# Kernel tuning notes

Measured on AMD Instinct MI355X. Metric: run time of the kernel, lower is better.

The kernel has to match this reference:

```python
import jax, jax.numpy as jnp
import numpy as np

B, F, V, E = 16384, 20, 100000, 32
D_BOT = F * E            # 640
DIMS = (512, 256)        # bottom MLP dims
TDIMS = (128, 64)        # tower hidden dims
N_DOM = 4


def setup_inputs() -> dict:
    key = jax.random.key(0)
    ks = jax.random.split(key, 16)
    inp = {
        "feature_ids": jax.random.randint(ks[0], (B, F), 0, V, dtype=jnp.int64),
        "domain_id": jax.random.randint(ks[1], (B,), 0, N_DOM, dtype=jnp.int64),
        # embedding tables [F, V, E]
        "emb": jax.random.normal(ks[2], (F, V, E), dtype=jnp.float32) * 0.01,
        # bottom MLP: 640 -> 512 -> 256 (relu, no output layer)
        "W1": jax.random.normal(ks[3], (D_BOT, DIMS[0]), dtype=jnp.float32) * (1.0 / np.sqrt(D_BOT)),
        "b1": jnp.zeros((DIMS[0],), dtype=jnp.float32),
        "W2": jax.random.normal(ks[4], (DIMS[0], DIMS[1]), dtype=jnp.float32) * (1.0 / np.sqrt(DIMS[0])),
        "b2": jnp.zeros((DIMS[1],), dtype=jnp.float32),
        # towers (stacked over domain dim): 256 -> 128 -> 64 -> 1
        "TW1": jax.random.normal(ks[5], (N_DOM, DIMS[1], TDIMS[0]), dtype=jnp.float32) * (1.0 / np.sqrt(DIMS[1])),
        "Tb1": jnp.zeros((N_DOM, TDIMS[0]), dtype=jnp.float32),
        "TW2": jax.random.normal(ks[6], (N_DOM, TDIMS[0], TDIMS[1]), dtype=jnp.float32) * (1.0 / np.sqrt(TDIMS[0])),
        "Tb2": jnp.zeros((N_DOM, TDIMS[1]), dtype=jnp.float32),
        "TW3": jax.random.normal(ks[7], (N_DOM, TDIMS[1], 1), dtype=jnp.float32) * (1.0 / np.sqrt(TDIMS[1])),
        "Tb3": jnp.zeros((N_DOM, 1), dtype=jnp.float32),
    }
    return inp


def reference(feature_ids, domain_id, emb, W1, b1, W2, b2, TW1, Tb1, TW2, Tb2, TW3, Tb3):
    # Embedding lookup + concat: [B, F, E] -> [B, F*E]
    e = emb[jnp.arange(F)[None, :], feature_ids]          # [B, F, E]
    h = e.reshape(B, F * E)
    # Shared bottom MLP (relu)
    h = jax.nn.relu(h @ W1 + b1)                          # [B, 512]
    h = jax.nn.relu(h @ W2 + b2)                          # [B, 256]
    # All domain towers computed densely for every sample (faithful to source)
    t = jax.nn.relu(jnp.einsum('bi,dio->bdo', h, TW1) + Tb1[None])   # [B, D, 128]
    t = jax.nn.relu(jnp.einsum('bdi,dio->bdo', t, TW2) + Tb2[None])  # [B, D, 64]
    logit = jnp.einsum('bdi,dio->bdo', t, TW3) + Tb3[None]           # [B, D, 1]
    ys = jax.nn.sigmoid(logit)[..., 0]                    # [B, D]
    # Select per-sample domain output via mask (domains are exclusive)
    onehot = jax.nn.one_hot(domain_id, N_DOM, dtype=ys.dtype)        # [B, D]
    final = jnp.sum(ys * onehot, axis=1)                  # [B]
    return final
```

## Files before the change

### kernel.cpp

```cpp
#include <hip/hip_runtime.h>

#define B_SZ  16384
#define F_SZ  20
#define V_SZ  100000
#define E_SZ  32
#define DBOT  640
#define D1    512
#define D2    256
#define T1D   128
#define T2D   64
#define NDOM  4

typedef __bf16 bf16x8 __attribute__((ext_vector_type(8)));
typedef float  f32x4  __attribute__((ext_vector_type(4)));

#define MFMA(a, b, c) __builtin_amdgcn_mfma_f32_16x16x32_bf16((a), (b), (c), 0, 0, 0)

__global__ __launch_bounds__(256) void k_prep(const float* __restrict__ W1,
                                              const float* __restrict__ W2,
                                              const float* __restrict__ TW1,
                                              const float* __restrict__ TW2,
                                              __bf16* __restrict__ W1P,
                                              __bf16* __restrict__ W2P,
                                              __bf16* __restrict__ TW1P,
                                              __bf16* __restrict__ TW2P,
                                              int* __restrict__ cnt) {
  int bid = blockIdx.x, tid = threadIdx.x;
  const float* src; __bf16* dst; int n, k, N;
  if (bid < 160) {
    long g = (long)bid * 256 + tid;
    int lane = g & 63; int kkg = (int)((g >> 6) % 20); int ntile = (int)(g / 1280);
    n = ntile * 16 + (lane & 15); k = kkg * 32 + ((lane >> 4) << 3);
    src = W1; N = D1; dst = W1P + g * 8;
  } else if (bid < 224) {
    long g = (long)(bid - 160) * 256 + tid;
    int lane = g & 63; int kkg = (int)((g >> 6) & 15); int ntile = (int)(g >> 10);
    n = ntile * 16 + (lane & 15); k = kkg * 32 + ((lane >> 4) << 3);
    src = W2; N = D2; dst = W2P + g * 8;
  } else if (bid < 288) {
    long g = (long)(bid - 224) * 256 + tid;
    int d = (int)(g >> 12); long r = g & 4095;
    int lane = r & 63; int kkg = (int)((r >> 6) & 7); int ntile = (int)(r >> 9);
    n = ntile * 16 + (lane & 15); k = kkg * 32 + ((lane >> 4) << 3);
    src = TW1 + (long)d * D2 * T1D; N = T1D;
    dst = TW1P + ((long)(d * 64 + ntile * 8 + kkg) * 64 + lane) * 8;
  } else if (bid < 304) {
    long g = (long)(bid - 288) * 256 + tid;
    int d = (int)(g >> 10); long r = g & 1023;
    int lane = r & 63; int kkg = (int)((r >> 6) & 3); int ntile = (int)(r >> 8);
    n = ntile * 16 + (lane & 15); k = kkg * 32 + ((lane >> 4) << 3);
    src = TW2 + (long)d * T1D * T2D; N = T2D;
    dst = TW2P + ((long)(d * 16 + ntile * 4 + kkg) * 64 + lane) * 8;
  } else {
    if (tid < NDOM) cnt[tid] = 0;
    return;
  }
  bf16x8 o;
#pragma unroll
  for (int e = 0; e < 8; ++e) o[e] = (__bf16)src[(long)(k + e) * N + n];
  *(bf16x8*)dst = o;
}

__global__ __launch_bounds__(512) void k_fused(const int* __restrict__ fids,
                                               const int* __restrict__ dom,
                                               const float* __restrict__ emb,
                                               const __bf16* __restrict__ W1P,
                                               const float* __restrict__ b1,
                                               const __bf16* __restrict__ W2P,
                                               const float* __restrict__ b2,
                                               __bf16* __restrict__ h2,
                                               int* __restrict__ cnt,
                                               int* __restrict__ lists) {
  __shared__ int   ids_lds[64 * F_SZ];
  __shared__ __bf16 sA[2][64 * 64];
  __shared__ __bf16 h1[64 * D1];

  int bid = blockIdx.x, tid = threadIdx.x;
  int lane = tid & 63, w = tid >> 6;
  int lrow = lane & 15, kq = lane >> 4;
  int m0 = bid * 64;

  if (bid < 64 && tid < 256) {
    int i = bid * 256 + tid;
    int d = dom[i];
    int pl = tid & 63;
#pragma unroll
    for (int dd = 0; dd < NDOM; ++dd) {
      unsigned long long md = __ballot(d == dd);
      if (d == dd) {
        int myoff = __popcll(md & ((1ull << pl) - 1ull));
        int leader = __ffsll((long long)md) - 1;
        int base = 0;
        if (pl == leader) base = atomicAdd(&cnt[dd], __popcll(md));
        base = __shfl(base, leader);
        lists[dd * B_SZ + base + myoff] = i;
      }
    }
  }

  for (int i = tid; i < 64 * F_SZ; i += 512) ids_lds[i] = fids[m0 * F_SZ + i];
  __syncthreads();

  int srow = tid >> 3, sc = tid & 7;
  int sbyte = srow * 128 + ((sc ^ (srow & 7)) << 4);

  float4 g0, g1;
  {
    int f = sc >> 2;
    int id = ids_lds[srow * F_SZ + f];
    const float* p = emb + ((long)f * V_SZ + id) * E_SZ + ((sc & 3) << 3);
    g0 = *(const float4*)p; g1 = *(const float4*)(p + 4);
  }

  f32x4 acc[4][4] = {};

  for (int s = 0; s < 10; ++s) {
    bf16x8 o;
    o[0] = (__bf16)g0.x; o[1] = (__bf16)g0.y; o[2] = (__bf16)g0.z; o[3] = (__bf16)g0.w;
    o[4] = (__bf16)g1.x; o[5] = (__bf16)g1.y; o[6] = (__bf16)g1.z; o[7] = (__bf16)g1.w;
    *(bf16x8*)((char*)&sA[s & 1][0] + sbyte) = o;
    if (s < 9) {
      int f = 2 * (s + 1) + (sc >> 2);
      int id = ids_lds[srow * F_SZ + f];
      const float* p = emb + ((long)f * V_SZ + id) * E_SZ + ((sc & 3) << 3);
      g0 = *(const float4*)p; g1 = *(const float4*)(p + 4);
    }
    __syncthreads();

    const char* sAb = (const char*)&sA[s & 1][0];
#pragma unroll
    for (int kk = 0; kk < 2; ++kk) {
      bf16x8 af[4];
#pragma unroll
      for (int mi = 0; mi < 4; ++mi) {
        int byte = ((mi * 16 + lrow) * 128 + (kk * 32 + kq * 8) * 2) ^ ((lrow & 7) << 4);
        af[mi] = *(const bf16x8*)(sAb + byte);
      }
#pragma unroll
      for (int ni = 0; ni < 4; ++ni) {
        bf16x8 bfr = *(const bf16x8*)(W1P +
            ((long)((w * 4 + ni) * 20 + (s * 2 + kk)) * 64 + lane) * 8);
#pragma unroll
        for (int mi = 0; mi < 4; ++mi)
          acc[mi][ni] = MFMA(af[mi], bfr, acc[mi][ni]);
      }
    }
  }

#pragma unroll
  for (int ni = 0; ni < 4; ++ni) {
    int col = w * 64 + ni * 16 + lrow;
    float bv = b1[col];
#pragma unroll
    for (int mi = 0; mi < 4; ++mi) {
#pragma unroll
      for (int r = 0; r < 4; ++r) {
        int row = mi * 16 + kq * 4 + r;
        float v = acc[mi][ni][r] + bv;
        v = v > 0.f ? v : 0.f;
        int byte = (row * 1024 + col * 2) ^ ((row & 7) << 4);
        *(__bf16*)((char*)h1 + byte) = (__bf16)v;
      }
    }
  }
  __syncthreads();

  f32x4 acc2[4][2] = {};
  for (int kkg = 0; kkg < 16; ++kkg) {
    bf16x8 a2[4];
#pragma unroll
    for (int mi = 0; mi < 4; ++mi) {
      int byte = ((mi * 16 + lrow) * 1024 + kkg * 64 + kq * 16) ^ ((lrow & 7) << 4);
      a2[mi] = *(const bf16x8*)((const char*)h1 + byte);
    }
#pragma unroll
    for (int ni = 0; ni < 2; ++ni) {
      bf16x8 bfr = *(const bf16x8*)(W2P +
          ((long)((w * 2 + ni) * 16 + kkg) * 64 + lane) * 8);
#pragma unroll
      for (int mi = 0; mi < 4; ++mi)
        acc2[mi][ni] = MFMA(a2[mi], bfr, acc2[mi][ni]);
    }
  }

#pragma unroll
  for (int ni = 0; ni < 2; ++ni) {
    int col = w * 32 + ni * 16 + lrow;
    float bv = b2[col];
#pragma unroll
    for (int mi = 0; mi < 4; ++mi) {
#pragma unroll
      for (int r = 0; r < 4; ++r) {
        long row = m0 + mi * 16 + kq * 4 + r;
        float v = acc2[mi][ni][r] + bv;
        v = v > 0.f ? v : 0.f;
        h2[row * D2 + col] = (__bf16)v;
      }
    }
  }
}

__global__ __launch_bounds__(256) void k_tower(const __bf16* __restrict__ h2,
                                               const __bf16* __restrict__ TW1P,
                                               const __bf16* __restrict__ TW2P,
                                               const float* __restrict__ Tb1,
                                               const float* __restrict__ Tb2,
                                               const float* __restrict__ TW3,
                                               const float* __restrict__ Tb3,
                                               const int* __restrict__ cnt,
                                               const int* __restrict__ lists,
                                               float* __restrict__ out) {
  __shared__ __bf16 t_lds[4][16 * 128];
  int d  = blockIdx.y;
  int nc = cnt[d];
  int base = blockIdx.x * 64;
  if (base >= nc) return;

  int tid  = threadIdx.x;
  int lane = tid & 63;
  int w    = tid >> 6;
  int row  = lane & 15;
  int kq   = lane >> 4;
  int slot = base + w * 16 + row;
  bool valid = slot < nc;
  int m0r = lists[d * B_SZ + (valid ? slot : 0)];

  bf16x8 a1[8];
#pragma unroll
  for (int kk = 0; kk < 8; ++kk)
    a1[kk] = *(const bf16x8*)(h2 + (long)m0r * D2 + kk * 32 + kq * 8);

  f32x4 acc1[8] = {};
#pragma unroll
  for (int kk = 0; kk < 8; ++kk) {
#pragma unroll
    for (int ni = 0; ni < 8; ++ni) {
      bf16x8 b = *(const bf16x8*)(TW1P +
          ((long)(d * 64 + ni * 8 + kk) * 64 + lane) * 8);
      acc1[ni] = MFMA(a1[kk], b, acc1[ni]);
    }
  }
#pragma unroll
  for (int ni = 0; ni < 8; ++ni) {
    float bv = Tb1[d * T1D + ni * 16 + row];
#pragma unroll
    for (int r = 0; r < 4; ++r) {
      float v = acc1[ni][r] + bv;
      v = v > 0.f ? v : 0.f;
      t_lds[w][(kq * 4 + r) * 128 + ni * 16 + row] = (__bf16)v;
    }
  }
  asm volatile("s_waitcnt lgkmcnt(0)" ::: "memory");

  bf16x8 a2[4];
#pragma unroll
  for (int kk = 0; kk < 4; ++kk)
    a2[kk] = *(const bf16x8*)(&t_lds[w][row * 128 + kk * 32 + kq * 8]);
  f32x4 acc2[4] = {};
#pragma unroll
  for (int kk = 0; kk < 4; ++kk) {
#pragma unroll
    for (int ni = 0; ni < 4; ++ni) {
      bf16x8 b = *(const bf16x8*)(TW2P +
          ((long)(d * 16 + ni * 4 + kk) * 64 + lane) * 8);
      acc2[ni] = MFMA(a2[kk], b, acc2[ni]);
    }
  }
  asm volatile("s_waitcnt lgkmcnt(0)" ::: "memory");
#pragma unroll
  for (int ni = 0; ni < 4; ++ni) {
    float bv = Tb2[d * T2D + ni * 16 + row];
#pragma unroll
    for (int r = 0; r < 4; ++r) {
      float v = acc2[ni][r] + bv;
      v = v > 0.f ? v : 0.f;
      t_lds[w][(kq * 4 + r) * 64 + ni * 16 + row] = (__bf16)v;
    }
  }
  asm volatile("s_waitcnt lgkmcnt(0)" ::: "memory");

  float s = 0.f;
#pragma unroll
  for (int j = 0; j < 16; ++j)
    s += (float)t_lds[w][row * 64 + kq * 16 + j] * TW3[d * T2D + kq * 16 + j];
  s += __shfl_xor(s, 16);
  s += __shfl_xor(s, 32);
  s += Tb3[d];
  if (valid && kq == 0)
    out[m0r] = 1.0f / (1.0f + expf(-s));
}

extern "C" void kernel_launch(void* const* d_in, const int* in_sizes, int n_in,
                              void* d_out, int out_size, void* d_ws, size_t ws_size,
                              hipStream_t stream) {
  const int*   fids = (const int*)d_in[0];
  const int*   dom  = (const int*)d_in[1];
  const float* emb  = (const float*)d_in[2];
  const float* W1   = (const float*)d_in[3];
  const float* b1   = (const float*)d_in[4];
  const float* W2   = (const float*)d_in[5];
  const float* b2   = (const float*)d_in[6];
  const float* TW1  = (const float*)d_in[7];
  const float* Tb1  = (const float*)d_in[8];
  const float* TW2  = (const float*)d_in[9];
  const float* Tb2  = (const float*)d_in[10];
  const float* TW3  = (const float*)d_in[11];
  const float* Tb3  = (const float*)d_in[12];
  float* out = (float*)d_out;

  char* ws = (char*)d_ws;
  __bf16* W1P   = (__bf16*)(ws);
  __bf16* W2P   = (__bf16*)(ws + 655360);
  __bf16* TW1P  = (__bf16*)(ws + 917504);
  __bf16* TW2P  = (__bf16*)(ws + 1179648);
  __bf16* h2    = (__bf16*)(ws + 1245184);
  int*    lists = (int*)(ws + 9633792);
  int*    cnt   = (int*)(ws + 9895936);

  k_prep<<<305, 256, 0, stream>>>(W1, W2, TW1, TW2, W1P, W2P, TW1P, TW2P, cnt);

  k_fused<<<256, 512, 0, stream>>>(fids, dom, emb, W1P, b1, W2P, b2, h2,
                                   cnt, lists);

  k_tower<<<dim3(80, NDOM), 256, 0, stream>>>(h2, TW1P, TW2P, Tb1, Tb2,
                                              TW3, Tb3, cnt, lists, out);
}
```

Measured before the change: 54.94 us.

## Merge prep, bottom MLP and tower kernels into one persistent kernel with grid barriers

Replaces three kernel launches with a single 256-block kernel that runs weight packing and domain bucketing, then the bottom MLP, then the towers, separated by software grid barriers built on atomics. It also double-buffers the embedding gather registers so loads run two steps ahead, and swaps __syncthreads for a raw s_barrier. The aim is to remove launch gaps and kernel-boundary drains. In exchange it relies on all 256 blocks being co-resident for the spin barrier, and the tower phase now has only 64 blocks per domain looping over chunks. The barrier counter is reset by the same memset that clears cnt, so it starts at zero on each call.

```diff
diff --git a/kernel.cpp b/kernel.cpp
--- a/kernel.cpp
+++ b/kernel.cpp
@@ -16,278 +16,301 @@
 
 #define MFMA(a, b, c) __builtin_amdgcn_mfma_f32_16x16x32_bf16((a), (b), (c), 0, 0, 0)
 
-__global__ __launch_bounds__(256) void k_prep(const float* __restrict__ W1,
+__device__ __forceinline__ void grid_barrier(int* bar) {
+  __syncthreads();
+  if (threadIdx.x == 0) {
+    __threadfence();
+    atomicAdd(bar, 1);
+    while (__hip_atomic_load(bar, __ATOMIC_ACQUIRE, __HIP_MEMORY_SCOPE_AGENT) < 256) {
+      __builtin_amdgcn_s_sleep(2);
+    }
+    __threadfence();
+  }
+  __syncthreads();
+}
+
+__global__ __launch_bounds__(512) void k_mono(const int* __restrict__ fids,
+                                              const int* __restrict__ dom,
+                                              const float* __restrict__ emb,
+                                              const float* __restrict__ W1,
+                                              const float* __restrict__ b1,
                                               const float* __restrict__ W2,
+                                              const float* __restrict__ b2,
                                               const float* __restrict__ TW1,
+                                              const float* __restrict__ Tb1,
                                               const float* __restrict__ TW2,
+                                              const float* __restrict__ Tb2,
+                                              const float* __restrict__ TW3,
+                                              const float* __restrict__ Tb3,
                                               __bf16* __restrict__ W1P,
                                               __bf16* __restrict__ W2P,
                                               __bf16* __restrict__ TW1P,
                                               __bf16* __restrict__ TW2P,
-                                              int* __restrict__ cnt) {
-  int bid = blockIdx.x, tid = threadIdx.x;
-  const float* src; __bf16* dst; int n, k, N;
-  if (bid < 160) {
-    long g = (long)bid * 256 + tid;
-    int lane = g & 63; int kkg = (int)((g >> 6) % 20); int ntile = (int)(g / 1280);
-    n = ntile * 16 + (lane & 15); k = kkg * 32 + ((lane >> 4) << 3);
-    src = W1; N = D1; dst = W1P + g * 8;
-  } else if (bid < 224) {
-    long g = (long)(bid - 160) * 256 + tid;
-    int lane = g & 63; int kkg = (int)((g >> 6) & 15); int ntile = (int)(g >> 10);
-    n = ntile * 16 + (lane & 15); k = kkg * 32 + ((lane >> 4) << 3);
-    src = W2; N = D2; dst = W2P + g * 8;
-  } else if (bid < 288) {
-    long g = (long)(bid - 224) * 256 + tid;
-    int d = (int)(g >> 12); long r = g & 4095;
-    int lane = r & 63; int kkg = (int)((r >> 6) & 7); int ntile = (int)(r >> 9);
-    n = ntile * 16 + (lane & 15); k = kkg * 32 + ((lane >> 4) << 3);
-    src = TW1 + (long)d * D2 * T1D; N = T1D;
-    dst = TW1P + ((long)(d * 64 + ntile * 8 + kkg) * 64 + lane) * 8;
-  } else if (bid < 304) {
-    long g = (long)(bid - 288) * 256 + tid;
-    int d = (int)(g >> 10); long r = g & 1023;
-    int lane = r & 63; int kkg = (int)((r >> 6) & 3); int ntile = (int)(r >> 8);
-    n = ntile * 16 + (lane & 15); k = kkg * 32 + ((lane >> 4) << 3);
-    src = TW2 + (long)d * T1D * T2D; N = T2D;
-    dst = TW2P + ((long)(d * 16 + ntile * 4 + kkg) * 64 + lane) * 8;
-  } else {
-    if (tid < NDOM) cnt[tid] = 0;
-    return;
-  }
-  bf16x8 o;
-#pragma unroll
-  for (int e = 0; e < 8; ++e) o[e] = (__bf16)src[(long)(k + e) * N + n];
-  *(bf16x8*)dst = o;
-}
-
-__global__ __launch_bounds__(512) void k_fused(const int* __restrict__ fids,
-                                               const int* __restrict__ dom,
-                                               const float* __restrict__ emb,
-                                               const __bf16* __restrict__ W1P,
-                                               const float* __restrict__ b1,
-                                               const __bf16* __restrict__ W2P,
-                                               const float* __restrict__ b2,
-                                               __bf16* __restrict__ h2,
-                                               int* __restrict__ cnt,
-                                               int* __restrict__ lists) {
-  __shared__ int   ids_lds[64 * F_SZ];
-  __shared__ __bf16 sA[2][64 * 64];
-  __shared__ __bf16 h1[64 * D1];
+                                              __bf16* __restrict__ h2,
+                                              int* __restrict__ lists,
+                                              int* __restrict__ cnt,
+                                              int* __restrict__ bar,
+                                              float* __restrict__ out) {
+  __shared__ __attribute__((aligned(16))) char smem[87040];
+  int*    ids_lds = (int*)smem;
+  __bf16* sA      = (__bf16*)(smem + 5120);
+  __bf16* h1      = (__bf16*)(smem + 21504);
+  __bf16* t_lds   = (__bf16*)smem;
 
   int bid = blockIdx.x, tid = threadIdx.x;
   int lane = tid & 63, w = tid >> 6;
   int lrow = lane & 15, kq = lane >> 4;
-  int m0 = bid * 64;
-
-  if (bid < 64 && tid < 256) {
-    int i = bid * 256 + tid;
-    int d = dom[i];
-    int pl = tid & 63;
-#pragma unroll
-    for (int dd = 0; dd < NDOM; ++dd) {
-      unsigned long long md = __ballot(d == dd);
-      if (d == dd) {
-        int myoff = __popcll(md & ((1ull << pl) - 1ull));
-        int leader = __ffsll((long long)md) - 1;
-        int base = 0;
-        if (pl == leader) base = atomicAdd(&cnt[dd], __popcll(md));
-        base = __shfl(base, leader);
-        lists[dd * B_SZ + base + myoff] = i;
+
+  {
+    int t = bid * 512 + tid;
+    if (t < 77824) {
+      const float* src; __bf16* dst; int n, k, N;
+      if (t < 40960) {
+        int g = t;
+        int l = g & 63, kkg = (g >> 6) % 20, ntile = g / 1280;
+        n = ntile * 16 + (l & 15); k = kkg * 32 + ((l >> 4) << 3);
+        src = W1; N = D1; dst = W1P + (long)g * 8;
+      } else if (t < 57344) {
+        int g = t - 40960;
+        int l = g & 63, kkg = (g >> 6) & 15, ntile = g >> 10;
+        n = ntile * 16 + (l & 15); k = kkg * 32 + ((l >> 4) << 3);
+        src = W2; N = D2; dst = W2P + (long)g * 8;
+      } else if (t < 73728) {
+        int g = t - 57344;
+        int d = g >> 12, r = g & 4095;
+        int l = r & 63, kkg = (r >> 6) & 7, ntile = r >> 9;
+        n = ntile * 16 + (l & 15); k = kkg * 32 + ((l >> 4) << 3);
+        src = TW1 + (long)d * D2 * T1D; N = T1D;
+        dst = TW1P + ((long)(d * 64 + ntile * 8 + kkg) * 64 + l) * 8;
+      } else {
+        int g = t - 73728;
+        int d = g >> 10, r = g & 1023;
+        int l = r & 63, kkg = (r >> 6) & 3, ntile = r >> 8;
+        n = ntile * 16 + (l & 15); k = kkg * 32 + ((l >> 4) << 3);
+        src = TW2 + (long)d * T1D * T2D; N = T2D;
+        dst = TW2P + ((long)(d * 16 + ntile * 4 + kkg) * 64 + l) * 8;
+      }
+      bf16x8 o;
+#pragma unroll
+      for (int e = 0; e < 8; ++e) o[e] = (__bf16)src[(long)(k + e) * N + n];
+      *(bf16x8*)dst = o;
+    } else if (t < 94208) {
+      int i = t - 77824;
+      int d = dom[i];
+      int pl = tid & 63;
+#pragma unroll
+      for (int dd = 0; dd < NDOM; ++dd) {
+        unsigned long long md = __ballot(d == dd);
+        if (d == dd) {
+          int myoff = __popcll(md & ((1ull << pl) - 1ull));
+          int leader = __ffsll((long long)md) - 1;
+          int base = 0;
+          if (pl == leader) base = atomicAdd(&cnt[dd], __popcll(md));
+          base = __shfl(base, leader);
+          lists[dd * B_SZ + base + myoff] = i;
+        }
       }
     }
   }
-
-  for (int i = tid; i < 64 * F_SZ; i += 512) ids_lds[i] = fids[m0 * F_SZ + i];
-  __syncthreads();
-
-  int srow = tid >> 3, sc = tid & 7;
-  int sbyte = srow * 128 + ((sc ^ (srow & 7)) << 4);
-
-  float4 g0, g1;
+  grid_barrier(&bar[0]);
+
   {
-    int f = sc >> 2;
-    int id = ids_lds[srow * F_SZ + f];
-    const float* p = emb + ((long)f * V_SZ + id) * E_SZ + ((sc & 3) << 3);
-    g0 = *(const float4*)p; g1 = *(const float4*)(p + 4);
-  }
-
-  f32x4 acc[4][4] = {};
-
-  for (int s = 0; s < 10; ++s) {
-    bf16x8 o;
-    o[0] = (__bf16)g0.x; o[1] = (__bf16)g0.y; o[2] = (__bf16)g0.z; o[3] = (__bf16)g0.w;
-    o[4] = (__bf16)g1.x; o[5] = (__bf16)g1.y; o[6] = (__bf16)g1.z; o[7] = (__bf16)g1.w;
-    *(bf16x8*)((char*)&sA[s & 1][0] + sbyte) = o;
-    if (s < 9) {
-      int f = 2 * (s + 1) + (sc >> 2);
+    int m0 = bid * 64;
+    for (int i = tid; i < 64 * F_SZ; i += 512) ids_lds[i] = fids[m0 * F_SZ + i];
+    __syncthreads();
+
+    int srow = tid >> 3, sc = tid & 7;
+    int sbyte = srow * 128 + ((sc ^ (srow & 7)) << 4);
+
+    float4 g0a, g1a, g0b, g1b;
+    {
+      int f = 0 + (sc >> 2);
       int id = ids_lds[srow * F_SZ + f];
       const float* p = emb + ((long)f * V_SZ + id) * E_SZ + ((sc & 3) << 3);
-      g0 = *(const float4*)p; g1 = *(const float4*)(p + 4);
-    }
-    __syncthreads();
-
-    const char* sAb = (const char*)&sA[s & 1][0];
-#pragma unroll
-    for (int kk = 0; kk < 2; ++kk) {
-      bf16x8 af[4];
+      g0a = *(const float4*)p; g1a = *(const float4*)(p + 4);
+    }
+    {
+      int f = 2 + (sc >> 2);
+      int id = ids_lds[srow * F_SZ + f];
+      const float* p = emb + ((long)f * V_SZ + id) * E_SZ + ((sc & 3) << 3);
+      g0b = *(const float4*)p; g1b = *(const float4*)(p + 4);
+    }
+
+    f32x4 acc[4][4] = {};
+
+#define GSTEP(S, G0, G1)                                                     \
+    {                                                                        \
+      bf16x8 o;                                                              \
+      o[0]=(__bf16)G0.x; o[1]=(__bf16)G0.y; o[2]=(__bf16)G0.z; o[3]=(__bf16)G0.w; \
+      o[4]=(__bf16)G1.x; o[5]=(__bf16)G1.y; o[6]=(__bf16)G1.z; o[7]=(__bf16)G1.w; \
+      *(bf16x8*)((char*)(sA + ((S) & 1) * 4096) + sbyte) = o;                \
+      if ((S) + 2 < 10) {      \
+        int f = 2 * ((S) + 2) + (sc >> 2);                                   \
+        int id = ids_lds[srow * F_SZ + f];                                   \
+        const float* p = emb + ((long)f * V_SZ + id) * E_SZ + ((sc & 3) << 3); \
+        G0 = *(const float4*)p; G1 = *(const float4*)(p + 4);                \
+      }                                                                      \
+         \
+      asm volatile("s_waitcnt lgkmcnt(0)" ::: "memory");                     \
+      __builtin_amdgcn_s_barrier();                                          \
+      const char* sAb = (const char*)(sA + ((S) & 1) * 4096);                \
+      _Pragma("unroll")                                                      \
+      for (int kk = 0; kk < 2; ++kk) {                                       \
+        bf16x8 af[4];                                                        \
+        _Pragma("unroll")                                                    \
+        for (int mi = 0; mi < 4; ++mi) {                                     \
+          int byte = ((mi * 16 + lrow) * 128 + (kk * 32 + kq * 8) * 2) ^ ((lrow & 7) << 4); \
+          af[mi] = *(const bf16x8*)(sAb + byte);                             \
+        }                                                                    \
+        _Pragma("unroll")                                                    \
+        for (int ni = 0; ni < 4; ++ni) {                                     \
+          bf16x8 bfr = *(const bf16x8*)(W1P +                                \
+              ((long)((w * 4 + ni) * 20 + ((S) * 2 + kk)) * 64 + lane) * 8); \
+          _Pragma("unroll")                                                  \
+          for (int mi = 0; mi < 4; ++mi)                                     \
+            acc[mi][ni] = MFMA(af[mi], bfr, acc[mi][ni]);                    \
+        }                                                                    \
+      }                                                                      \
+    }
+
+    for (int ss = 0; ss < 5; ++ss) {
+      GSTEP(2 * ss,     g0a, g1a)
+      GSTEP(2 * ss + 1, g0b, g1b)
+    }
+#undef GSTEP
+
+#pragma unroll
+    for (int ni = 0; ni < 4; ++ni) {
+      int col = w * 64 + ni * 16 + lrow;
+      float bv = b1[col];
 #pragma unroll
       for (int mi = 0; mi < 4; ++mi) {
-        int byte = ((mi * 16 + lrow) * 128 + (kk * 32 + kq * 8) * 2) ^ ((lrow & 7) << 4);
-        af[mi] = *(const bf16x8*)(sAb + byte);
-      }
+#pragma unroll
+        for (int r = 0; r < 4; ++r) {
+          int row = mi * 16 + kq * 4 + r;
+          float v = acc[mi][ni][r] + bv;
+          v = v > 0.f ? v : 0.f;
+          int byte = (row * 1024 + col * 2) ^ ((row & 7) << 4);
+          *(__bf16*)((char*)h1 + byte) = (__bf16)v;
+        }
+      }
+    }
+    asm volatile("s_waitcnt lgkmcnt(0)" ::: "memory");
+    __builtin_amdgcn_s_barrier();
+
+    f32x4 acc2[4][2] = {};
+    for (int kkg = 0; kkg < 16; ++kkg) {
+      bf16x8 a2[4];
+#pragma unroll
+      for (int mi = 0; mi < 4; ++mi) {
+        int byte = ((mi * 16 + lrow) * 1024 + kkg * 64 + kq * 16) ^ ((lrow & 7) << 4);
+        a2[mi] = *(const bf16x8*)((const char*)h1 + byte);
+      }
+#pragma unroll
+      for (int ni = 0; ni < 2; ++ni) {
+        bf16x8 bfr = *(const bf16x8*)(W2P +
+            ((long)((w * 2 + ni) * 16 + kkg) * 64 + lane) * 8);
+#pragma unroll
+        for (int mi = 0; mi < 4; ++mi)
+          acc2[mi][ni] = MFMA(a2[mi], bfr, acc2[mi][ni]);
+      }
+    }
+
+#pragma unroll
+    for (int ni = 0; ni < 2; ++ni) {
+      int col = w * 32 + ni * 16 + lrow;
+      float bv = b2[col];
+#pragma unroll
+      for (int mi = 0; mi < 4; ++mi) {
+#pragma unroll
+        for (int r = 0; r < 4; ++r) {
+          long row = m0 + mi * 16 + kq * 4 + r;
+          float v = acc2[mi][ni][r] + bv;
+          v = v > 0.f ? v : 0.f;
+          h2[row * D2 + col] = (__bf16)v;
+        }
+      }
+    }
+  }
+  grid_barrier(&bar[1]);
+
+  {
+    int d = bid >> 6;
+    int chunk = bid & 63;
+    int nc = cnt[d];
+    __bf16* tw = t_lds + w * 2048;
+    int row = lrow;
+
+    for (int base = chunk * 128; base < nc; base += 64 * 128) {
+      int slot = base + w * 16 + row;
+      bool valid = slot < nc;
+      int m0r = lists[d * B_SZ + (valid ? slot : 0)];
+
+      bf16x8 a1[8];
+#pragma unroll
+      for (int kk = 0; kk < 8; ++kk)
+        a1[kk] = *(const bf16x8*)(h2 + (long)m0r * D2 + kk * 32 + kq * 8);
+
+      f32x4 acc1[8] = {};
+#pragma unroll
+      for (int kk = 0; kk < 8; ++kk) {
+#pragma unroll
+        for (int ni = 0; ni < 8; ++ni) {
+          bf16x8 b = *(const bf16x8*)(TW1P +
+              ((long)(d * 64 + ni * 8 + kk) * 64 + lane) * 8);
+          acc1[ni] = MFMA(a1[kk], b, acc1[ni]);
+        }
+      }
+#pragma unroll
+      for (int ni = 0; ni < 8; ++ni) {
+        float bv = Tb1[d * T1D + ni * 16 + row];
+#pragma unroll
+        for (int r = 0; r < 4; ++r) {
+          float v = acc1[ni][r] + bv;
+          v = v > 0.f ? v : 0.f;
+          tw[(kq * 4 + r) * 128 + ni * 16 + row] = (__bf16)v;
+        }
+      }
+      asm volatile("s_waitcnt lgkmcnt(0)" ::: "memory");
+
+      bf16x8 a2[4];
+#pragma unroll
+      for (int kk = 0; kk < 4; ++kk)
+        a2[kk] = *(const bf16x8*)(&tw[row * 128 + kk * 32 + kq * 8]);
+      f32x4 acc2[4] = {};
+#pragma unroll
+      for (int kk = 0; kk < 4; ++kk) {
+#pragma unroll
+        for (int ni = 0; ni < 4; ++ni) {
+          bf16x8 b = *(const bf16x8*)(TW2P +
+              ((long)(d * 16 + ni * 4 + kk) * 64 + lane) * 8);
+          acc2[ni] = MFMA(a2[kk], b, acc2[ni]);
+        }
+      }
+      asm volatile("s_waitcnt lgkmcnt(0)" ::: "memory");
 #pragma unroll
       for (int ni = 0; ni < 4; ++ni) {
-        bf16x8 bfr = *(const bf16x8*)(W1P +
-            ((long)((w * 4 + ni) * 20 + (s * 2 + kk)) * 64 + lane) * 8);
-#pragma unroll
-        for (int mi = 0; mi < 4; ++mi)
-          acc[mi][ni] = MFMA(af[mi], bfr, acc[mi][ni]);
-      }
+        float bv = Tb2[d * T2D + ni * 16 + row];
+#pragma unroll
+        for (int r = 0; r < 4; ++r) {
+          float v = acc2[ni][r] + bv;
+          v = v > 0.f ? v : 0.f;
+          tw[(kq * 4 + r) * 64 + ni * 16 + row] = (__bf16)v;
+        }
+      }
+      asm volatile("s_waitcnt lgkmcnt(0)" ::: "memory");
+
+      float s = 0.f;
+#pragma unroll
+      for (int j = 0; j < 16; ++j)
+        s += (float)tw[row * 64 + kq * 16 + j] * TW3[d * T2D + kq * 16 + j];
+      s += __shfl_xor(s, 16);
+      s += __shfl_xor(s, 32);
+      s += Tb3[d];
+      if (valid && kq == 0)
+        out[m0r] = 1.0f / (1.0f + expf(-s));
     }
   }
-
-#pragma unroll
-  for (int ni = 0; ni < 4; ++ni) {
-    int col = w * 64 + ni * 16 + lrow;
-    float bv = b1[col];
-#pragma unroll
-    for (int mi = 0; mi < 4; ++mi) {
-#pragma unroll
-      for (int r = 0; r < 4; ++r) {
-        int row = mi * 16 + kq * 4 + r;
-        float v = acc[mi][ni][r] + bv;
-        v = v > 0.f ? v : 0.f;
-        int byte = (row * 1024 + col * 2) ^ ((row & 7) << 4);
-        *(__bf16*)((char*)h1 + byte) = (__bf16)v;
-      }
-    }
-  }
-  __syncthreads();
-
-  f32x4 acc2[4][2] = {};
-  for (int kkg = 0; kkg < 16; ++kkg) {
-    bf16x8 a2[4];
-#pragma unroll
-    for (int mi = 0; mi < 4; ++mi) {
-      int byte = ((mi * 16 + lrow) * 1024 + kkg * 64 + kq * 16) ^ ((lrow & 7) << 4);
-      a2[mi] = *(const bf16x8*)((const char*)h1 + byte);
-    }
-#pragma unroll
-    for (int ni = 0; ni < 2; ++ni) {
-      bf16x8 bfr = *(const bf16x8*)(W2P +
-          ((long)((w * 2 + ni) * 16 + kkg) * 64 + lane) * 8);
-#pragma unroll
-      for (int mi = 0; mi < 4; ++mi)
-        acc2[mi][ni] = MFMA(a2[mi], bfr, acc2[mi][ni]);
-    }
-  }
-
-#pragma unroll
-  for (int ni = 0; ni < 2; ++ni) {
-    int col = w * 32 + ni * 16 + lrow;
-    float bv = b2[col];
-#pragma unroll
-    for (int mi = 0; mi < 4; ++mi) {
-#pragma unroll
-      for (int r = 0; r < 4; ++r) {
-        long row = m0 + mi * 16 + kq * 4 + r;
-        float v = acc2[mi][ni][r] + bv;
-        v = v > 0.f ? v : 0.f;
-        h2[row * D2 + col] = (__bf16)v;
-      }
-    }
-  }
-}
-
-__global__ __launch_bounds__(256) void k_tower(const __bf16* __restrict__ h2,
-                                               const __bf16* __restrict__ TW1P,
-                                               const __bf16* __restrict__ TW2P,
-                                               const float* __restrict__ Tb1,
-                                               const float* __restrict__ Tb2,
-                                               const float* __restrict__ TW3,
-                                               const float* __restrict__ Tb3,
-                                               const int* __restrict__ cnt,
-                                               const int* __restrict__ lists,
-                                               float* __restrict__ out) {
-  __shared__ __bf16 t_lds[4][16 * 128];
-  int d  = blockIdx.y;
-  int nc = cnt[d];
-  int base = blockIdx.x * 64;
-  if (base >= nc) return;
-
-  int tid  = threadIdx.x;
-  int lane = tid & 63;
-  int w    = tid >> 6;
-  int row  = lane & 15;
-  int kq   = lane >> 4;
-  int slot = base + w * 16 + row;
-  bool valid = slot < nc;
-  int m0r = lists[d * B_SZ + (valid ? slot : 0)];
-
-  bf16x8 a1[8];
-#pragma unroll
-  for (int kk = 0; kk < 8; ++kk)
-    a1[kk] = *(const bf16x8*)(h2 + (long)m0r * D2 + kk * 32 + kq * 8);
-
-  f32x4 acc1[8] = {};
-#pragma unroll
-  for (int kk = 0; kk < 8; ++kk) {
-#pragma unroll
-    for (int ni = 0; ni < 8; ++ni) {
-      bf16x8 b = *(const bf16x8*)(TW1P +
-          ((long)(d * 64 + ni * 8 + kk) * 64 + lane) * 8);
-      acc1[ni] = MFMA(a1[kk], b, acc1[ni]);
-    }
-  }
-#pragma unroll
-  for (int ni = 0; ni < 8; ++ni) {
-    float bv = Tb1[d * T1D + ni * 16 + row];
-#pragma unroll
-    for (int r = 0; r < 4; ++r) {
-      float v = acc1[ni][r] + bv;
-      v = v > 0.f ? v : 0.f;
-      t_lds[w][(kq * 4 + r) * 128 + ni * 16 + row] = (__bf16)v;
-    }
-  }
-  asm volatile("s_waitcnt lgkmcnt(0)" ::: "memory");
-
-  bf16x8 a2[4];
-#pragma unroll
-  for (int kk = 0; kk < 4; ++kk)
-    a2[kk] = *(const bf16x8*)(&t_lds[w][row * 128 + kk * 32 + kq * 8]);
-  f32x4 acc2[4] = {};
-#pragma unroll
-  for (int kk = 0; kk < 4; ++kk) {
-#pragma unroll
-    for (int ni = 0; ni < 4; ++ni) {
-      bf16x8 b = *(const bf16x8*)(TW2P +
-          ((long)(d * 16 + ni * 4 + kk) * 64 + lane) * 8);
-      acc2[ni] = MFMA(a2[kk], b, acc2[ni]);
-    }
-  }
-  asm volatile("s_waitcnt lgkmcnt(0)" ::: "memory");
-#pragma unroll
-  for (int ni = 0; ni < 4; ++ni) {
-    float bv = Tb2[d * T2D + ni * 16 + row];
-#pragma unroll
-    for (int r = 0; r < 4; ++r) {
-      float v = acc2[ni][r] + bv;
-      v = v > 0.f ? v : 0.f;
-      t_lds[w][(kq * 4 + r) * 64 + ni * 16 + row] = (__bf16)v;
-    }
-  }
-  asm volatile("s_waitcnt lgkmcnt(0)" ::: "memory");
-
-  float s = 0.f;
-#pragma unroll
-  for (int j = 0; j < 16; ++j)
-    s += (float)t_lds[w][row * 64 + kq * 16 + j] * TW3[d * T2D + kq * 16 + j];
-  s += __shfl_xor(s, 16);
-  s += __shfl_xor(s, 32);
-  s += Tb3[d];
-  if (valid && kq == 0)
-    out[m0r] = 1.0f / (1.0f + expf(-s));
 }
 
 extern "C" void kernel_launch(void* const* d_in, const int* in_sizes, int n_in,
@@ -316,12 +339,12 @@
   __bf16* h2    = (__bf16*)(ws + 1245184);
   int*    lists = (int*)(ws + 9633792);
   int*    cnt   = (int*)(ws + 9895936);
-
-  k_prep<<<305, 256, 0, stream>>>(W1, W2, TW1, TW2, W1P, W2P, TW1P, TW2P, cnt);
-
-  k_fused<<<256, 512, 0, stream>>>(fids, dom, emb, W1P, b1, W2P, b2, h2,
-                                   cnt, lists);
-
-  k_tower<<<dim3(80, NDOM), 256, 0, stream>>>(h2, TW1P, TW2P, Tb1, Tb2,
-                                              TW3, Tb3, cnt, lists, out);
+  int*    bar   = (int*)(ws + 9895952);
+
+  hipMemsetAsync(cnt, 0, 32, stream);
+
+  k_mono<<<256, 512, 0, stream>>>(fids, dom, emb, W1, b1, W2, b2,
+                                  TW1, Tb1, TW2, Tb2, TW3, Tb3,
+                                  W1P, W2P, TW1P, TW2P, h2, lists, cnt, bar,
+                                  out);
 }
```

Result: slower. 115.5 us (+110.2%).

## Deepen embedding gather prefetch and register double-buffer W1 fragments

Applied to the files above, without the earlier changes.

Restructures the first GEMM loop into a fully unrolled macro body that prefetches embedding rows two stages ahead and double-buffers the W1 B-fragments in registers, loading the next stage's weights after the current MFMAs. It replaces __syncthreads with an explicit lgkmcnt wait, a raw barrier and a sched_barrier, and adds a launch-bounds minimum of 2 blocks per CU. The aim is to hide global gather and weight-load latency behind MFMA work. The extra live registers and the occupancy hint may force spills or constrain scheduling.

```diff
diff --git a/kernel.cpp b/kernel.cpp
--- a/kernel.cpp
+++ b/kernel.cpp
@@ -61,17 +61,17 @@
   *(bf16x8*)dst = o;
 }
 
-__global__ __launch_bounds__(512) void k_fused(const int* __restrict__ fids,
-                                               const int* __restrict__ dom,
-                                               const float* __restrict__ emb,
-                                               const __bf16* __restrict__ W1P,
-                                               const float* __restrict__ b1,
-                                               const __bf16* __restrict__ W2P,
-                                               const float* __restrict__ b2,
-                                               __bf16* __restrict__ h2,
-                                               int* __restrict__ cnt,
-                                               int* __restrict__ lists) {
-  __shared__ int   ids_lds[64 * F_SZ];
+__global__ __launch_bounds__(512, 2) void k_fused(const int* __restrict__ fids,
+                                                  const int* __restrict__ dom,
+                                                  const float* __restrict__ emb,
+                                                  const __bf16* __restrict__ W1P,
+                                                  const float* __restrict__ b1,
+                                                  const __bf16* __restrict__ W2P,
+                                                  const float* __restrict__ b2,
+                                                  __bf16* __restrict__ h2,
+                                                  int* __restrict__ cnt,
+                                                  int* __restrict__ lists) {
+  __shared__ int    ids_lds[64 * F_SZ];
   __shared__ __bf16 sA[2][64 * 64];
   __shared__ __bf16 h1[64 * D1];
 
@@ -103,49 +103,81 @@
 
   int srow = tid >> 3, sc = tid & 7;
   int sbyte = srow * 128 + ((sc ^ (srow & 7)) << 4);
-
-  float4 g0, g1;
+  int fsub = sc >> 2, esub = (sc & 3) << 3;
+
+  float4 g0a, g1a, g0b, g1b;
   {
-    int f = sc >> 2;
-    int id = ids_lds[srow * F_SZ + f];
-    const float* p = emb + ((long)f * V_SZ + id) * E_SZ + ((sc & 3) << 3);
-    g0 = *(const float4*)p; g1 = *(const float4*)(p + 4);
-  }
+    int id = ids_lds[srow * F_SZ + fsub];
+    const float* p = emb + ((long)fsub * V_SZ + id) * E_SZ + esub;
+    g0a = *(const float4*)p; g1a = *(const float4*)(p + 4);
+  }
+  {
+    int id = ids_lds[srow * F_SZ + 2 + fsub];
+    const float* p = emb + ((long)(2 + fsub) * V_SZ + id) * E_SZ + esub;
+    g0b = *(const float4*)p; g1b = *(const float4*)(p + 4);
+  }
+  bf16x8 bfA[8], bfB[8];
+#pragma unroll
+  for (int ni = 0; ni < 4; ++ni)
+#pragma unroll
+    for (int kk = 0; kk < 2; ++kk)
+      bfA[ni * 2 + kk] = *(const bf16x8*)(W1P +
+          ((long)((w * 4 + ni) * 20 + kk) * 64 + lane) * 8);
 
   f32x4 acc[4][4] = {};
 
-  for (int s = 0; s < 10; ++s) {
-    bf16x8 o;
-    o[0] = (__bf16)g0.x; o[1] = (__bf16)g0.y; o[2] = (__bf16)g0.z; o[3] = (__bf16)g0.w;
-    o[4] = (__bf16)g1.x; o[5] = (__bf16)g1.y; o[6] = (__bf16)g1.z; o[7] = (__bf16)g1.w;
-    *(bf16x8*)((char*)&sA[s & 1][0] + sbyte) = o;
-    if (s < 9) {
-      int f = 2 * (s + 1) + (sc >> 2);
-      int id = ids_lds[srow * F_SZ + f];
-      const float* p = emb + ((long)f * V_SZ + id) * E_SZ + ((sc & 3) << 3);
-      g0 = *(const float4*)p; g1 = *(const float4*)(p + 4);
-    }
-    __syncthreads();
-
-    const char* sAb = (const char*)&sA[s & 1][0];
-#pragma unroll
-    for (int kk = 0; kk < 2; ++kk) {
-      bf16x8 af[4];
-#pragma unroll
-      for (int mi = 0; mi < 4; ++mi) {
-        int byte = ((mi * 16 + lrow) * 128 + (kk * 32 + kq * 8) * 2) ^ ((lrow & 7) << 4);
-        af[mi] = *(const bf16x8*)(sAb + byte);
-      }
-#pragma unroll
-      for (int ni = 0; ni < 4; ++ni) {
-        bf16x8 bfr = *(const bf16x8*)(W1P +
-            ((long)((w * 4 + ni) * 20 + (s * 2 + kk)) * 64 + lane) * 8);
-#pragma unroll
-        for (int mi = 0; mi < 4; ++mi)
-          acc[mi][ni] = MFMA(af[mi], bfr, acc[mi][ni]);
-      }
-    }
-  }
+#define BODY(S, G0, G1, BC, BN)                                              \
+    {                                                                        \
+      bf16x8 o;                                                              \
+      o[0]=(__bf16)G0.x; o[1]=(__bf16)G0.y; o[2]=(__bf16)G0.z; o[3]=(__bf16)G0.w; \
+      o[4]=(__bf16)G1.x; o[5]=(__bf16)G1.y; o[6]=(__bf16)G1.z; o[7]=(__bf16)G1.w; \
+      *(bf16x8*)((char*)sA + ((S) & 1) * 8192 + sbyte) = o;                  \
+      asm volatile("s_waitcnt lgkmcnt(0)" ::: "memory");                     \
+      __builtin_amdgcn_s_barrier();                                          \
+      __builtin_amdgcn_sched_barrier(0);                                     \
+      const char* sAb = (const char*)sA + ((S) & 1) * 8192;                  \
+      bf16x8 af[2][4];                                                       \
+      _Pragma("unroll")                                                      \
+      for (int kk = 0; kk < 2; ++kk)                                         \
+        _Pragma("unroll")                                                    \
+        for (int mi = 0; mi < 4; ++mi) {                                     \
+          int byte = ((mi * 16 + lrow) * 128 + (kk * 32 + kq * 8) * 2) ^ ((lrow & 7) << 4); \
+          af[kk][mi] = *(const bf16x8*)(sAb + byte);                         \
+        }                                                                    \
+      _Pragma("unroll")                                                      \
+      for (int kk = 0; kk < 2; ++kk)                                         \
+        _Pragma("unroll")                                                    \
+        for (int ni = 0; ni < 4; ++ni)                                       \
+          _Pragma("unroll")                                                  \
+          for (int mi = 0; mi < 4; ++mi)                                     \
+            acc[mi][ni] = MFMA(af[kk][mi], BC[ni * 2 + kk], acc[mi][ni]);    \
+      if ((S) + 1 < 10) {   \
+        _Pragma("unroll")                                                    \
+        for (int ni = 0; ni < 4; ++ni)                                       \
+          _Pragma("unroll")                                                  \
+          for (int kk = 0; kk < 2; ++kk)                                     \
+            BN[ni * 2 + kk] = *(const bf16x8*)(W1P +                         \
+                ((long)((w * 4 + ni) * 20 + ((S) + 1) * 2 + kk) * 64 + lane) * 8); \
+      }                                                                      \
+      if ((S) + 2 < 10) {    \
+        int f = 2 * ((S) + 2) + fsub;                                        \
+        int id = ids_lds[srow * F_SZ + f];                                   \
+        const float* p = emb + ((long)f * V_SZ + id) * E_SZ + esub;          \
+        G0 = *(const float4*)p; G1 = *(const float4*)(p + 4);                \
+      }                                                                      \
+    }
+
+  BODY(0, g0a, g1a, bfA, bfB)
+  BODY(1, g0b, g1b, bfB, bfA)
+  BODY(2, g0a, g1a, bfA, bfB)
+  BODY(3, g0b, g1b, bfB, bfA)
+  BODY(4, g0a, g1a, bfA, bfB)
+  BODY(5, g0b, g1b, bfB, bfA)
+  BODY(6, g0a, g1a, bfA, bfB)
+  BODY(7, g0b, g1b, bfB, bfA)
+  BODY(8, g0a, g1a, bfA, bfB)
+  BODY(9, g0b, g1b, bfB, bfA)
+#undef BODY
 
 #pragma unroll
   for (int ni = 0; ni < 4; ++ni) {
```

New measurement: 50.88 us. 1.08x faster.

## Gather entire embedding tile into LDS upfront instead of double-buffered stages

Applied to the files above, without the earlier changes.

Replaces the 10-stage double-buffered embedding gather (one float4 pair per thread per stage, with a barrier each step) with a single bulk gather. Each thread issues all 10 of its gathers at once, and the full 64x640 bf16 A tile is stored in LDS before the first GEMM loop, which then runs without per-stage barriers. This exposes more memory-level parallelism for the random embedding reads and removes nine syncs. In exchange, LDS use grows from 16KB to 80KB for the A tile and register pressure rises from the 20 float4 held per thread, which could cut occupancy. It also adds an unroll-4 pragma on the second GEMM loop.

```diff
diff --git a/kernel.cpp b/kernel.cpp
--- a/kernel.cpp
+++ b/kernel.cpp
@@ -71,8 +71,8 @@
                                                __bf16* __restrict__ h2,
                                                int* __restrict__ cnt,
                                                int* __restrict__ lists) {
-  __shared__ int   ids_lds[64 * F_SZ];
-  __shared__ __bf16 sA[2][64 * 64];
+  __shared__ int    ids_lds[64 * F_SZ];
+  __shared__ __bf16 sA[64 * DBOT];
   __shared__ __bf16 h1[64 * D1];
 
   int bid = blockIdx.x, tid = threadIdx.x;
@@ -101,49 +101,49 @@
   for (int i = tid; i < 64 * F_SZ; i += 512) ids_lds[i] = fids[m0 * F_SZ + i];
   __syncthreads();
 
-  int srow = tid >> 3, sc = tid & 7;
-  int sbyte = srow * 128 + ((sc ^ (srow & 7)) << 4);
-
-  float4 g0, g1;
+  float4 ga[10], gb[10];
+  int sb[10];
   {
-    int f = sc >> 2;
-    int id = ids_lds[srow * F_SZ + f];
-    const float* p = emb + ((long)f * V_SZ + id) * E_SZ + ((sc & 3) << 3);
-    g0 = *(const float4*)p; g1 = *(const float4*)(p + 4);
-  }
+#pragma unroll
+    for (int i = 0; i < 10; ++i) {
+      unsigned c = tid + i * 512;
+      unsigned row = c / 80;
+      unsigned cc = c - row * 80;
+      int f = cc >> 2, es = (cc & 3) << 3;
+      int id = ids_lds[row * F_SZ + f];
+      const float* p = emb + ((long)f * V_SZ + id) * E_SZ + es;
+      ga[i] = *(const float4*)p;
+      gb[i] = *(const float4*)(p + 4);
+      sb[i] = (int)(row * 1280 + cc * 16) ^ ((row & 7) << 4);
+    }
+#pragma unroll
+    for (int i = 0; i < 10; ++i) {
+      bf16x8 o;
+      o[0] = (__bf16)ga[i].x; o[1] = (__bf16)ga[i].y;
+      o[2] = (__bf16)ga[i].z; o[3] = (__bf16)ga[i].w;
+      o[4] = (__bf16)gb[i].x; o[5] = (__bf16)gb[i].y;
+      o[6] = (__bf16)gb[i].z; o[7] = (__bf16)gb[i].w;
+      *(bf16x8*)((char*)sA + sb[i]) = o;
+    }
+  }
+  __syncthreads();
 
   f32x4 acc[4][4] = {};
-
-  for (int s = 0; s < 10; ++s) {
-    bf16x8 o;
-    o[0] = (__bf16)g0.x; o[1] = (__bf16)g0.y; o[2] = (__bf16)g0.z; o[3] = (__bf16)g0.w;
-    o[4] = (__bf16)g1.x; o[5] = (__bf16)g1.y; o[6] = (__bf16)g1.z; o[7] = (__bf16)g1.w;
-    *(bf16x8*)((char*)&sA[s & 1][0] + sbyte) = o;
-    if (s < 9) {
-      int f = 2 * (s + 1) + (sc >> 2);
-      int id = ids_lds[srow * F_SZ + f];
-      const float* p = emb + ((long)f * V_SZ + id) * E_SZ + ((sc & 3) << 3);
-      g0 = *(const float4*)p; g1 = *(const float4*)(p + 4);
-    }
-    __syncthreads();
-
-    const char* sAb = (const char*)&sA[s & 1][0];
-#pragma unroll
-    for (int kk = 0; kk < 2; ++kk) {
-      bf16x8 af[4];
-#pragma unroll
-      for (int mi = 0; mi < 4; ++mi) {
-        int byte = ((mi * 16 + lrow) * 128 + (kk * 32 + kq * 8) * 2) ^ ((lrow & 7) << 4);
-        af[mi] = *(const bf16x8*)(sAb + byte);
-      }
-#pragma unroll
-      for (int ni = 0; ni < 4; ++ni) {
-        bf16x8 bfr = *(const bf16x8*)(W1P +
-            ((long)((w * 4 + ni) * 20 + (s * 2 + kk)) * 64 + lane) * 8);
-#pragma unroll
-        for (int mi = 0; mi < 4; ++mi)
-          acc[mi][ni] = MFMA(af[mi], bfr, acc[mi][ni]);
-      }
+#pragma unroll
+  for (int f = 0; f < F_SZ; ++f) {
+    bf16x8 af[4];
+#pragma unroll
+    for (int mi = 0; mi < 4; ++mi) {
+      int byte = ((mi * 16 + lrow) * 1280 + (f * 32 + kq * 8) * 2) ^ ((lrow & 7) << 4);
+      af[mi] = *(const bf16x8*)((const char*)sA + byte);
+    }
+#pragma unroll
+    for (int ni = 0; ni < 4; ++ni) {
+      bf16x8 bfr = *(const bf16x8*)(W1P +
+          ((long)((w * 4 + ni) * 20 + f) * 64 + lane) * 8);
+#pragma unroll
+      for (int mi = 0; mi < 4; ++mi)
+        acc[mi][ni] = MFMA(af[mi], bfr, acc[mi][ni]);
     }
   }
 
@@ -166,6 +166,7 @@
   __syncthreads();
 
   f32x4 acc2[4][2] = {};
+#pragma unroll 4
   for (int kkg = 0; kkg < 16; ++kkg) {
     bf16x8 a2[4];
 #pragma unroll
@@ -318,10 +319,8 @@
   int*    cnt   = (int*)(ws + 9895936);
 
   k_prep<<<305, 256, 0, stream>>>(W1, W2, TW1, TW2, W1P, W2P, TW1P, TW2P, cnt);
-
   k_fused<<<256, 512, 0, stream>>>(fids, dom, emb, W1P, b1, W2P, b2, h2,
                                    cnt, lists);
-
   k_tower<<<dim3(80, NDOM), 256, 0, stream>>>(h2, TW1P, TW2P, Tb1, Tb2,
                                               TW3, Tb3, cnt, lists, out);
 }
```

After: 53.16 us. -3.2%, faster.
